# Performance work log

Measured on AMD Instinct MI355X. Metric: run time of the kernel, lower is better.

Reference implementation:

```python
import jax, jax.numpy as jnp
import numpy as np

B, S, HID = 4, 128, 4096
D, HQ, HK = 128, 32, 8
PAGES, PSIZE, NPP = 64, 256, 16  # page pool, page size, pages per sequence
THETA = 10000.0
EPS = 1e-6
SCALE = 1.0 / float(np.sqrt(D))


def setup_inputs() -> dict:
    key = jax.random.key(0)
    ks = jax.random.split(key, 10)
    x = jax.random.normal(ks[0], (B, S, HID), jnp.float32)
    Wq = jax.random.normal(ks[1], (HQ * D, HID), jnp.float32) * 0.02
    Wk = jax.random.normal(ks[2], (HK * D, HID), jnp.float32) * 0.02
    Wv = jax.random.normal(ks[3], (HK * D, HID), jnp.float32) * 0.02
    Wo = jax.random.normal(ks[4], (HID, HQ * D), jnp.float32) * 0.02
    q_norm_w = jax.random.uniform(ks[5], (D,), jnp.float32)
    k_norm_w = jax.random.uniform(ks[6], (D,), jnp.float32)
    k_cache = jax.random.normal(ks[7], (PAGES, PSIZE, HK, D), jnp.float32)
    v_cache = jax.random.normal(ks[8], (PAGES, PSIZE, HK, D), jnp.float32)
    block_table = jnp.arange(B * NPP, dtype=jnp.int32).reshape(B, NPP)
    cache_seqlens = jax.random.randint(ks[9], (B,), 0, 3800).astype(jnp.int32)
    return dict(x=x, Wq=Wq, Wk=Wk, Wv=Wv, Wo=Wo, q_norm_w=q_norm_w,
                k_norm_w=k_norm_w, k_cache=k_cache, v_cache=v_cache,
                block_table=block_table, cache_seqlens=cache_seqlens)


def _rmsnorm(t, w):
    # per-head RMSNorm over head_dim (constant_bias = 0)
    var = jnp.mean(t * t, axis=-1, keepdims=True)
    return t * jax.lax.rsqrt(var + EPS) * w


def _rope(t, pos):
    # NeoX-style half-rotation. t: [B,S,H,D], pos: [B,S]
    inv_freq = 1.0 / (THETA ** (jnp.arange(0, D, 2, dtype=jnp.float32) / D))  # [D/2]
    freqs = pos[..., None].astype(jnp.float32) * inv_freq                     # [B,S,D/2]
    cos = jnp.cos(freqs)[:, :, None, :]
    sin = jnp.sin(freqs)[:, :, None, :]
    t1, t2 = t[..., : D // 2], t[..., D // 2:]
    return jnp.concatenate([t1 * cos - t2 * sin, t2 * cos + t1 * sin], axis=-1)


def reference(x, Wq, Wk, Wv, Wo, q_norm_w, k_norm_w, k_cache, v_cache,
              block_table, cache_seqlens):
    bsz, seqlen, _ = x.shape
    # QKV projections
    q = jnp.einsum('bsd,ed->bse', x, Wq).reshape(bsz, seqlen, HQ, D)
    k = jnp.einsum('bsd,ed->bse', x, Wk).reshape(bsz, seqlen, HK, D)
    v = jnp.einsum('bsd,ed->bse', x, Wv).reshape(bsz, seqlen, HK, D)
    # QK-norm then RoPE (fused norm+rope path of the module)
    q = _rmsnorm(q, q_norm_w)
    k = _rmsnorm(k, k_norm_w)
    pos = cache_seqlens[:, None] + jnp.arange(seqlen)[None, :]  # [B,S]
    q = _rope(q, pos)
    k = _rope(k, pos)
    # Gather paged KV cache: [B, NPP*PSIZE, HK, D]
    L = NPP * PSIZE
    kc = k_cache[block_table].reshape(bsz, L, HK, D)
    vc = v_cache[block_table].reshape(bsz, L, HK, D)
    # Append new tokens (flash_attn_with_kvcache writes k,v into the cache)
    k_all = jnp.concatenate([kc, k], axis=1)  # [B, L+S, HK, D]
    v_all = jnp.concatenate([vc, v], axis=1)
    # Valid mask: cache slots < cache_seqlens; all new keys valid (causal=False, full window)
    valid_c = jnp.arange(L)[None, :] < cache_seqlens[:, None]          # [B, L]
    valid = jnp.concatenate(
        [valid_c, jnp.ones((bsz, seqlen), dtype=bool)], axis=1)        # [B, L+S]
    rep = HQ // HK
    k_all = jnp.repeat(k_all, rep, axis=2)
    v_all = jnp.repeat(v_all, rep, axis=2)
    scores = jnp.einsum('bqhd,bkhd->bhqk', q, k_all) * SCALE
    scores = jnp.where(valid[:, None, None, :], scores, -1e30)
    probs = jax.nn.softmax(scores, axis=-1)
    o = jnp.einsum('bhqk,bkhd->bqhd', probs, v_all)
    o = o.reshape(bsz, seqlen, HQ * D)
    return jnp.einsum('bse,de->bsd', o, Wo)
```

## Files before the change

### kernel.cpp

```cpp
#include <hip/hip_runtime.h>

typedef unsigned short u16;
typedef float f4v __attribute__((ext_vector_type(4)));
typedef short s8v __attribute__((ext_vector_type(8)));
typedef int   i4v __attribute__((ext_vector_type(4)));

#define SCALE_ 0.08838834764831845f
#define LOG2E_ 1.44269504088896340f

__device__ __forceinline__ u16 f2b(float f) {
    union { float f; unsigned u; } c; c.f = f;
    unsigned u = c.u + 0x7fffu + ((c.u >> 16) & 1u);
    return (u16)(u >> 16);
}

typedef const __attribute__((address_space(1))) unsigned int gu32;
typedef __attribute__((address_space(3))) unsigned int lu32;
__device__ __forceinline__ void glds16(const void* g, void* l) {
    __builtin_amdgcn_global_load_lds((gu32*)g, (lu32*)l, 16, 0, 0);
}

__device__ __forceinline__ int rho(int kv) {
    return (kv & 0x20) | ((kv & 0x04) << 2) | ((kv & 0x18) >> 1) | (kv & 3);
}

template <int RB>
__global__ __launch_bounds__(256) void wcvt_k(const float* __restrict__ src,
                                              u16* __restrict__ dst, int K) {
    const int kt = blockIdx.x, nt = blockIdx.y;
    u16* out = dst + ((size_t)nt * gridDim.x + kt) * (RB * 64);
#pragma unroll
    for (int i = 0; i < RB / 32; i++) {
        int c = threadIdx.x + i * 256;
        int r = c >> 3, c16 = c & 7, cc = c16 ^ (r & 7);
        const float* p = src + (size_t)(nt * RB + r) * K + kt * 64 + cc * 8;
        float4 f0 = *(const float4*)p, f1 = *(const float4*)(p + 4);
        s8v v;
        v[0] = (short)f2b(f0.x); v[1] = (short)f2b(f0.y);
        v[2] = (short)f2b(f0.z); v[3] = (short)f2b(f0.w);
        v[4] = (short)f2b(f1.x); v[5] = (short)f2b(f1.y);
        v[6] = (short)f2b(f1.z); v[7] = (short)f2b(f1.w);
        *(s8v*)(out + r * 64 + c16 * 8) = v;
    }
}

__global__ __launch_bounds__(256) void fgemm2(const u16* __restrict__ Ag,
                                              const u16* __restrict__ Bg,
                                              float* __restrict__ Cp,
                                              int M, int N, int K, int Ksl,
                                              int NY, int NZ) {
    __shared__ __align__(16) u16 As[2][4096];
    __shared__ __align__(16) u16 Bs[2][8192];
    const int tid = threadIdx.x, lane = tid & 63, wid = tid >> 6;
    const int lm = lane & 15, lg = lane >> 4;
    const int nb = gridDim.x, per = nb >> 3, w = blockIdx.x;
    const int idx = (w & 7) * per + (w >> 3);
    const int nx = idx / (NY * NZ);
    const int rem = idx - nx * (NY * NZ);
    const int my = rem % NY, z = rem / NY;
    const int m0 = my * 64, n0 = nx * 128;
    const int KT = K >> 6, NT = Ksl >> 6;
    const int kt0 = (z * Ksl) >> 6;
    const u16* ga = Ag + ((size_t)my * KT + kt0) * 4096;
    const u16* gb = Bg + ((size_t)nx * KT + kt0) * 8192;
    Cp += (size_t)z * M * N;

    f4v acc[4][2];
#pragma unroll
    for (int mi = 0; mi < 4; mi++)
#pragma unroll
        for (int ni = 0; ni < 2; ni++) acc[mi][ni] = (f4v){0.f, 0.f, 0.f, 0.f};

    auto STAGE = [&](int buf, int kt) {
        const char* a = (const char*)(ga + (size_t)kt * 4096) + tid * 16;
        const char* b = (const char*)(gb + (size_t)kt * 8192) + tid * 16;
        char* la = (char*)As[buf] + tid * 16;
        char* lb = (char*)Bs[buf] + tid * 16;
        glds16(a, la);
        glds16(a + 4096, la + 4096);
#pragma unroll
        for (int i = 0; i < 4; i++) glds16(b + i * 4096, lb + i * 4096);
    };

    STAGE(0, 0);
    asm volatile("s_waitcnt vmcnt(0)" ::: "memory");
    __syncthreads();

    for (int kt = 0; kt < NT; ++kt) {
        const int cur = kt & 1;
        if (kt + 1 < NT) STAGE(cur ^ 1, kt + 1);
#pragma unroll
        for (int ks = 0; ks < 2; ks++) {
            s8v av[4], bv[2];
#pragma unroll
            for (int mi = 0; mi < 4; mi++) {
                int r = mi * 16 + lm;
                av[mi] = *(const s8v*)(As[cur] + r * 64 + (((ks * 4 + lg) ^ (r & 7)) * 8));
            }
#pragma unroll
            for (int ni = 0; ni < 2; ni++) {
                int r = wid * 32 + ni * 16 + lm;
                bv[ni] = *(const s8v*)(Bs[cur] + r * 64 + (((ks * 4 + lg) ^ (r & 7)) * 8));
            }
#pragma unroll
            for (int mi = 0; mi < 4; mi++)
#pragma unroll
                for (int ni = 0; ni < 2; ni++)
                    acc[mi][ni] = __builtin_amdgcn_mfma_f32_16x16x32_bf16(av[mi], bv[ni], acc[mi][ni], 0, 0, 0);
        }
        asm volatile("s_waitcnt vmcnt(0)" ::: "memory");
        __syncthreads();
    }

#pragma unroll
    for (int mi = 0; mi < 4; mi++)
#pragma unroll
        for (int ni = 0; ni < 2; ni++)
#pragma unroll
            for (int r = 0; r < 4; r++) {
                int m = m0 + mi * 16 + lg * 4 + r;
                int n = n0 + wid * 32 + ni * 16 + lm;
                Cp[(size_t)m * N + n] = acc[mi][ni][r];
            }
}

__global__ __launch_bounds__(256) void nrope_k(const float* __restrict__ src,
                                               u16* __restrict__ dst,
                                               const float* __restrict__ w,
                                               const int* __restrict__ cseq,
                                               int nheads, float oscale,
                                               int nsl, size_t sls) {
    const int lane = threadIdx.x & 63;
    const int rid = blockIdx.x * 4 + (threadIdx.x >> 6);
    const int s = (rid / nheads) & 127;
    const int b = rid / (nheads * 128);
    const float* p = src + (size_t)rid * 128;
    float x1 = 0.f, x2 = 0.f;
    for (int sl = 0; sl < nsl; sl++) {
        x1 += p[sl * sls + lane];
        x2 += p[sl * sls + lane + 64];
    }
    float ss = x1 * x1 + x2 * x2;
#pragma unroll
    for (int off = 1; off < 64; off <<= 1) ss += __shfl_xor(ss, off);
    float inv = rsqrtf(ss * (1.0f / 128.0f) + 1e-6f);
    float n1 = x1 * inv * w[lane];
    float n2 = x2 * inv * w[lane + 64];
    float pos = (float)(cseq[b] + s);
    float ang = pos * powf(10000.0f, -(float)lane * (1.0f / 64.0f));
    float cs = cosf(ang), sn = sinf(ang);
    dst[(size_t)rid * 128 + lane]      = f2b((n1 * cs - n2 * sn) * oscale);
    dst[(size_t)rid * 128 + lane + 64] = f2b((n2 * cs + n1 * sn) * oscale);
}

__global__ __launch_bounds__(256) void cvt_bf16k(const float* __restrict__ s,
                                                 u16* __restrict__ d, int n4,
                                                 int nsl, size_t sls) {
    int i = blockIdx.x * blockDim.x + threadIdx.x;
    if (i < n4) {
        f4v f = (f4v){0.f, 0.f, 0.f, 0.f};
        for (int sl = 0; sl < nsl; sl++)
            f += *(const f4v*)(s + sl * sls + (size_t)i * 4);
        ushort4 o;
        o.x = f2b(f[0]); o.y = f2b(f[1]); o.z = f2b(f[2]); o.w = f2b(f[3]);
        ((ushort4*)d)[i] = o;
    }
}

__global__ __launch_bounds__(256) void red4_k(const float* __restrict__ p,
                                              float* __restrict__ out, int n4,
                                              size_t sls) {
    int i = blockIdx.x * blockDim.x + threadIdx.x;
    if (i < n4) {
        f4v s = (f4v){0.f, 0.f, 0.f, 0.f};
#pragma unroll
        for (int sl = 0; sl < 4; sl++)
            s += *(const f4v*)(p + sl * sls + (size_t)i * 4);
        *(f4v*)(out + (size_t)i * 4) = s;
    }
}

__global__ __launch_bounds__(256) void cvtkv_k(const float* __restrict__ kc,
                                               const float* __restrict__ vc,
                                               const u16* __restrict__ kb,
                                               const u16* __restrict__ vb,
                                               const int* __restrict__ btab,
                                               const int* __restrict__ cseq,
                                               u16* __restrict__ kb2,
                                               u16* __restrict__ vb2) {
    const int t = blockIdx.x, hk = blockIdx.y, b = blockIdx.z;
    const int tid = threadIdx.x;
    const int cl = cseq[b];
    if (t < 64 && t * 64 >= cl) return;
    u16* kout = kb2 + ((size_t)(b * 8 + hk) * 66 + t) * 8192;
    u16* vout = vb2 + ((size_t)(b * 8 + hk) * 66 + t) * 8192;

    if (t < 64) {
#pragma unroll
        for (int i = 0; i < 4; i++) {
            int c = tid + i * 256; int r = c >> 4, c16 = c & 15;
            int rs = rho(r);
            int cc = c16 ^ (rs & 7);
            int p = t * 64 + r;
            const float* src = kc + (((size_t)btab[b * 16 + (p >> 8)] * 256 + (p & 255)) * 8 + hk) * 128 + cc * 8;
            float4 f0 = *(const float4*)src, f1 = *(const float4*)(src + 4);
            s8v v;
            v[0] = (short)f2b(f0.x); v[1] = (short)f2b(f0.y); v[2] = (short)f2b(f0.z); v[3] = (short)f2b(f0.w);
            v[4] = (short)f2b(f1.x); v[5] = (short)f2b(f1.y); v[6] = (short)f2b(f1.z); v[7] = (short)f2b(f1.w);
            *(s8v*)(kout + rs * 128 + c16 * 8) = v;
        }
#pragma unroll
        for (int i = 0; i < 4; i++) {
            int c = tid + i * 256; int pr = c >> 5, c16v = c & 31;
            int nc = c16v ^ pr;
            int n = nc * 4;
            int p = t * 64 + pr * 2;
            const float* s0 = vc + (((size_t)btab[b * 16 + (p >> 8)] * 256 + (p & 255)) * 8 + hk) * 128 + n;
            float4 e = *(const float4*)s0, o = *(const float4*)(s0 + 1024);
            i4v w;
            w[0] = (int)((unsigned)f2b(e.x) | ((unsigned)f2b(o.x) << 16));
            w[1] = (int)((unsigned)f2b(e.y) | ((unsigned)f2b(o.y) << 16));
            w[2] = (int)((unsigned)f2b(e.z) | ((unsigned)f2b(o.z) << 16));
            w[3] = (int)((unsigned)f2b(e.w) | ((unsigned)f2b(o.w) << 16));
            *(i4v*)(vout + pr * 256 + c16v * 8) = w;
        }
    } else {
        int s0r = (t - 64) * 64;
#pragma unroll
        for (int i = 0; i < 4; i++) {
            int c = tid + i * 256; int r = c >> 4, c16 = c & 15;
            int rs = rho(r);
            int cc = c16 ^ (rs & 7);
            s8v v = *(const s8v*)(kb + ((size_t)(b * 128 + s0r + r) * 8 + hk) * 128 + cc * 8);
            *(s8v*)(kout + rs * 128 + c16 * 8) = v;
        }
#pragma unroll
        for (int i = 0; i < 4; i++) {
            int c = tid + i * 256; int pr = c >> 5, c16v = c & 31;
            int nc = c16v ^ pr;
            int n = nc * 4;
            const u16* s0 = vb + ((size_t)(b * 128 + s0r + pr * 2) * 8 + hk) * 128 + n;
            ushort4 e = *(const ushort4*)s0, o = *(const ushort4*)(s0 + 1024);
            i4v w;
            w[0] = (int)((unsigned)e.x | ((unsigned)o.x << 16));
            w[1] = (int)((unsigned)e.y | ((unsigned)o.y << 16));
            w[2] = (int)((unsigned)e.z | ((unsigned)o.z << 16));
            w[3] = (int)((unsigned)e.w | ((unsigned)o.w << 16));
            *(i4v*)(vout + pr * 256 + c16v * 8) = w;
        }
    }
}

__global__ __launch_bounds__(256) void fattn6_k(const u16* __restrict__ qb,
                                                const u16* __restrict__ kb2,
                                                const u16* __restrict__ vb2,
                                                const int* __restrict__ cseq,
                                                float* __restrict__ po,
                                                float* __restrict__ mb,
                                                float* __restrict__ lb) {
    __shared__ __align__(16) char Ks[2][8192];
    __shared__ __align__(16) char Vs[2][8192];

    const int tid = threadIdx.x, lane = tid & 63, wid = tid >> 6;
    const int lm = lane & 15, lg = lane >> 4;
    const int bid = blockIdx.x;
    const int sp = bid & 3, half = (bid >> 2) & 1, h = (bid >> 3) & 31, b = bid >> 8;
    const int hk = h >> 2;

    s8v qa[4];
    {
        const u16* qp = qb + ((size_t)((b * 128 + half * 64 + wid * 16 + lm) * 32 + h)) * 128 + lg * 8;
#pragma unroll
        for (int ks = 0; ks < 4; ks++) qa[ks] = *(const s8v*)(qp + ks * 32);
    }

    float m_run = -1e30f, l_run = 0.f;
    f4v acc[8];
#pragma unroll
    for (int dt = 0; dt < 8; dt++) acc[dt] = (f4v){0.f, 0.f, 0.f, 0.f};

    const int cl = cseq[b];
    const int ntc = (cl + 31) >> 5;
    const int tlo = (ntc * sp) >> 2, thi = (ntc * (sp + 1)) >> 2;
    const int ncache = thi - tlo;
    const int ntiles = ncache + (sp == 3 ? 4 : 0);

    const char* gk = (const char*)kb2 + (size_t)(b * 8 + hk) * 66 * 16384;
    const char* gv = (const char*)vb2 + (size_t)(b * 8 + hk) * 66 * 16384;

    auto STAGE = [&](int buf, int gt) {
        const char* gkt = gk + (size_t)gt * 8192 + tid * 16;
        const char* gvt = gv + (size_t)gt * 8192 + tid * 16;
        char* lk = Ks[buf] + tid * 16;
        char* lv = Vs[buf] + tid * 16;
        glds16(gkt, lk);
        glds16(gkt + 4096, lk + 4096);
        glds16(gvt, lv);
        glds16(gvt + 4096, lv + 4096);
    };
    auto GT = [&](int ii) { return ii < ncache ? tlo + ii : 128 + (ii - ncache); };

    if (ntiles > 0) STAGE(0, GT(0));
    asm volatile("s_waitcnt vmcnt(0)" ::: "memory");
    __syncthreads();

    for (int ii = 0; ii < ntiles; ++ii) {
        const int cur = ii & 1;
        if (ii + 1 < ntiles) STAGE(cur ^ 1, GT(ii + 1));
        const int gt = GT(ii);
        const int t0 = gt * 32;

        f4v sc[2];
#pragma unroll
        for (int ct = 0; ct < 2; ct++) sc[ct] = (f4v){0.f, 0.f, 0.f, 0.f};
        __builtin_amdgcn_s_setprio(1);
#pragma unroll
        for (int ct = 0; ct < 2; ct++) {
#pragma unroll
            for (int ks = 0; ks < 4; ks++) {
                int r = ct * 16 + lm;
                s8v kf = *(const s8v*)(Ks[cur] + ((r * 256 + ks * 64 + lg * 16) ^ ((r & 7) << 4)));
                sc[ct] = __builtin_amdgcn_mfma_f32_16x16x32_bf16(kf, qa[ks], sc[ct], 0, 0, 0);
            }
        }
        __builtin_amdgcn_s_setprio(0);

        if (gt < 128 && (t0 + 32 > cl)) {
#pragma unroll
            for (int ct = 0; ct < 2; ct++)
#pragma unroll
                for (int r = 0; r < 4; r++) {
                    int kvloc = lg * 8 + ct * 4 + r;
                    if (t0 + kvloc >= cl) sc[ct][r] = -1e30f;
                }
        }

        float mt = fmaxf(fmaxf(fmaxf(sc[0][0], sc[0][1]), fmaxf(sc[0][2], sc[0][3])),
                         fmaxf(fmaxf(sc[1][0], sc[1][1]), fmaxf(sc[1][2], sc[1][3])));
        mt = fmaxf(mt, __shfl_xor(mt, 16));
        mt = fmaxf(mt, __shfl_xor(mt, 32));

        if (__any(mt > m_run + 12.0f)) {
            float mn = fmaxf(m_run, mt);
            float corr = exp2f(m_run - mn);
            m_run = mn;
            l_run *= corr;
            float c0 = __shfl(corr, lg * 4 + 0);
            float c1 = __shfl(corr, lg * 4 + 1);
            float c2 = __shfl(corr, lg * 4 + 2);
            float c3 = __shfl(corr, lg * 4 + 3);
#pragma unroll
            for (int dt = 0; dt < 8; dt++) {
                acc[dt][0] *= c0; acc[dt][1] *= c1;
                acc[dt][2] *= c2; acc[dt][3] *= c3;
            }
        }

        short pb[2][4];
        float ladd = 0.f;
#pragma unroll
        for (int ct = 0; ct < 2; ct++)
#pragma unroll
            for (int r = 0; r < 4; r++) {
                float pv = exp2f(sc[ct][r] - m_run);
                ladd += pv;
                pb[ct][r] = (short)f2b(pv);
            }
        l_run += ladd;

        __builtin_amdgcn_s_setprio(1);
        {
            s8v pa;
#pragma unroll
            for (int j = 0; j < 4; j++) { pa[j] = pb[0][j]; pa[4 + j] = pb[1][j]; }
            const int pko = (gt & 1) << 4;
#pragma unroll
            for (int dt = 0; dt < 8; dt++) {
                i4v vv;
#pragma unroll
                for (int t = 0; t < 4; t++) {
                    int p = lg * 4 + t;
                    vv[t] = *(const int*)(Vs[cur] + p * 512 + ((((dt * 16 + lm) * 4)) ^ (((p + pko) & 31) << 4)));
                }
                union { i4v i; s8v s; } u; u.i = vv;
                acc[dt] = __builtin_amdgcn_mfma_f32_16x16x32_bf16(pa, u.s, acc[dt], 0, 0, 0);
            }
        }
        __builtin_amdgcn_s_setprio(0);

        asm volatile("s_waitcnt vmcnt(0)" ::: "memory");
        __syncthreads();
    }

#pragma unroll
    for (int dt = 0; dt < 8; dt++) {
#pragma unroll
        for (int r = 0; r < 4; r++) {
            int row = wid * 16 + lg * 4 + r;
            po[((size_t)bid * 64 + row) * 128 + dt * 16 + lm] = acc[dt][r];
        }
    }
    float lt = l_run;
    lt += __shfl_xor(lt, 16);
    lt += __shfl_xor(lt, 32);
    if (lg == 0) {
        mb[(size_t)bid * 64 + wid * 16 + lm] = m_run;
        lb[(size_t)bid * 64 + wid * 16 + lm] = lt;
    }
}

__global__ __launch_bounds__(256) void fcomb_k(const float* __restrict__ po,
                                               const float* __restrict__ mb,
                                               const float* __restrict__ lb,
                                               u16* __restrict__ obT) {
    const int pid = blockIdx.x, t = threadIdx.x;
    const int row = t >> 2, dq = t & 3;
    const int half = pid & 1, h = (pid >> 1) & 31, b = pid >> 6;
    float m[4], l[4];
#pragma unroll
    for (int i = 0; i < 4; i++) {
        m[i] = mb[(size_t)(pid * 4 + i) * 64 + row];
        l[i] = lb[(size_t)(pid * 4 + i) * 64 + row];
    }
    float M = fmaxf(fmaxf(m[0], m[1]), fmaxf(m[2], m[3]));
    float w[4], L = 0.f;
#pragma unroll
    for (int i = 0; i < 4; i++) { w[i] = exp2f(m[i] - M); L += w[i] * l[i]; }
    float invL = 1.0f / L;
    const int arow = b * 128 + half * 64 + row;
    const int mt = arow >> 6, rr = arow & 63;
#pragma unroll
    for (int j = 0; j < 8; j++) {
        f4v s = (f4v){0.f, 0.f, 0.f, 0.f};
#pragma unroll
        for (int i = 0; i < 4; i++) {
            f4v a = *(const f4v*)(po + ((size_t)(pid * 4 + i) * 64 + row) * 128 + dq * 32 + j * 4);
            s += w[i] * a;
        }
        ushort4 o;
        o.x = f2b(s[0] * invL); o.y = f2b(s[1] * invL);
        o.z = f2b(s[2] * invL); o.w = f2b(s[3] * invL);
        const int acol = h * 128 + dq * 32 + j * 4;
        const int kt = acol >> 6, cch = (acol >> 3) & 7, wo = acol & 7;
        *(ushort4*)(obT + ((size_t)(mt * 64 + kt)) * 4096 + rr * 64 + ((cch ^ (rr & 7)) * 8) + wo) = o;
    }
}

extern "C" void kernel_launch(void* const* d_in, const int* in_sizes, int n_in,
                              void* d_out, int out_size, void* d_ws, size_t ws_size,
                              hipStream_t stream) {
    const float* x   = (const float*)d_in[0];
    const float* Wq  = (const float*)d_in[1];
    const float* Wk  = (const float*)d_in[2];
    const float* Wv  = (const float*)d_in[3];
    const float* Wo  = (const float*)d_in[4];
    const float* qnw = (const float*)d_in[5];
    const float* knw = (const float*)d_in[6];
    const float* kc  = (const float*)d_in[7];
    const float* vc  = (const float*)d_in[8];
    const int* btab  = (const int*)d_in[9];
    const int* cseq  = (const int*)d_in[10];
    float* out = (float*)d_out;

    char* ws = (char*)d_ws;
    u16*   qb   = (u16*)(ws + 0);
    u16*   kb   = (u16*)(ws + 4194304);
    u16*   vb   = (u16*)(ws + 5242880);
    u16*   obT  = (u16*)(ws + 6291456);
    u16*   xb   = (u16*)(ws + 6291456);
    float* mbuf = (float*)(ws + 10485760);
    float* lbuf = (float*)(ws + 10747904);
    float* P    = (float*)(ws + 11010048);
    u16*   wW   = (u16*)(ws + 44564480);
    u16*   kb2  = (u16*)(ws + 44564480);
    u16*   vb2  = (u16*)(ws + 79167488);

    dim3 blk(256, 1, 1);
    const size_t slsQ = (size_t)512 * 4096, slsKV = (size_t)512 * 1024;

    wcvt_k<64><<<dim3(64, 8, 1), blk, 0, stream>>>(x, xb, 4096);

    wcvt_k<128><<<dim3(64, 32, 1), blk, 0, stream>>>(Wq, wW, 4096);
    fgemm2<<<dim3(1024, 1, 1), blk, 0, stream>>>(xb, wW, P, 512, 4096, 4096, 1024, 8, 4);
    nrope_k<<<dim3(4096, 1, 1), blk, 0, stream>>>(P, qb, qnw, cseq, 32, SCALE_ * LOG2E_, 4, slsQ);

    wcvt_k<128><<<dim3(64, 8, 1), blk, 0, stream>>>(Wk, wW, 4096);
    fgemm2<<<dim3(512, 1, 1), blk, 0, stream>>>(xb, wW, P, 512, 1024, 4096, 512, 8, 8);
    nrope_k<<<dim3(1024, 1, 1), blk, 0, stream>>>(P, kb, knw, cseq, 8, 1.0f, 8, slsKV);

    wcvt_k<128><<<dim3(64, 8, 1), blk, 0, stream>>>(Wv, wW, 4096);
    fgemm2<<<dim3(512, 1, 1), blk, 0, stream>>>(xb, wW, P, 512, 1024, 4096, 512, 8, 8);
    cvt_bf16k<<<dim3(512, 1, 1), blk, 0, stream>>>(P, vb, 131072, 8, slsKV);

    cvtkv_k<<<dim3(66, 8, 4), blk, 0, stream>>>(kc, vc, kb, vb, btab, cseq, kb2, vb2);
    fattn6_k<<<dim3(1024, 1, 1), blk, 0, stream>>>(qb, kb2, vb2, cseq, P, mbuf, lbuf);
    fcomb_k<<<dim3(256, 1, 1), blk, 0, stream>>>(P, mbuf, lbuf, obT);

    wcvt_k<128><<<dim3(64, 32, 1), blk, 0, stream>>>(Wo, wW, 4096);
    fgemm2<<<dim3(1024, 1, 1), blk, 0, stream>>>(obT, wW, P, 512, 4096, 4096, 1024, 8, 4);
    red4_k<<<dim3(2048, 1, 1), blk, 0, stream>>>(P, out, 2097152, slsQ);
}
```

Before: 259.6 us.

## Fuse Q/K/V projections into one GEMM with merged weight convert and epilogue

Merges the three separate weight conversions into one kernel that writes Wq, Wk and Wv into a single concatenated bf16 buffer. A single split-K GEMM with N=6144 then produces Q, K and V together, using 2 K-slices instead of 4 or 8, which cuts the partial-sum traffic. One epilogue kernel applies RMSNorm+RoPE to Q and K and converts V, replacing three launches. This reduces kernel launches and fp32 partial writes, at the cost of changing the grid/split-K balance of the GEMM and needing more workspace for the wider output.

```diff
diff --git a/kernel.cpp b/kernel.cpp
--- a/kernel.cpp
+++ b/kernel.cpp
@@ -34,6 +34,32 @@
         int c = threadIdx.x + i * 256;
         int r = c >> 3, c16 = c & 7, cc = c16 ^ (r & 7);
         const float* p = src + (size_t)(nt * RB + r) * K + kt * 64 + cc * 8;
+        float4 f0 = *(const float4*)p, f1 = *(const float4*)(p + 4);
+        s8v v;
+        v[0] = (short)f2b(f0.x); v[1] = (short)f2b(f0.y);
+        v[2] = (short)f2b(f0.z); v[3] = (short)f2b(f0.w);
+        v[4] = (short)f2b(f1.x); v[5] = (short)f2b(f1.y);
+        v[6] = (short)f2b(f1.z); v[7] = (short)f2b(f1.w);
+        *(s8v*)(out + r * 64 + c16 * 8) = v;
+    }
+}
+
+__global__ __launch_bounds__(256) void wcvt3_k(const float* __restrict__ Wq,
+                                               const float* __restrict__ Wk,
+                                               const float* __restrict__ Wv,
+                                               u16* __restrict__ dst, int K) {
+    const int kt = blockIdx.x, nt = blockIdx.y;
+    const float* src;
+    int ln;
+    if (nt < 32)      { src = Wq; ln = nt; }
+    else if (nt < 40) { src = Wk; ln = nt - 32; }
+    else              { src = Wv; ln = nt - 40; }
+    u16* out = dst + ((size_t)nt * gridDim.x + kt) * 8192;
+#pragma unroll
+    for (int i = 0; i < 4; i++) {
+        int c = threadIdx.x + i * 256;
+        int r = c >> 3, c16 = c & 7, cc = c16 ^ (r & 7);
+        const float* p = src + (size_t)(ln * 128 + r) * K + kt * 64 + cc * 8;
         float4 f0 = *(const float4*)p, f1 = *(const float4*)(p + 4);
         s8v v;
         v[0] = (short)f2b(f0.x); v[1] = (short)f2b(f0.y);
@@ -124,46 +150,62 @@
             }
 }
 
-__global__ __launch_bounds__(256) void nrope_k(const float* __restrict__ src,
-                                               u16* __restrict__ dst,
-                                               const float* __restrict__ w,
-                                               const int* __restrict__ cseq,
-                                               int nheads, float oscale,
-                                               int nsl, size_t sls) {
-    const int lane = threadIdx.x & 63;
-    const int rid = blockIdx.x * 4 + (threadIdx.x >> 6);
-    const int s = (rid / nheads) & 127;
-    const int b = rid / (nheads * 128);
-    const float* p = src + (size_t)rid * 128;
-    float x1 = 0.f, x2 = 0.f;
-    for (int sl = 0; sl < nsl; sl++) {
-        x1 += p[sl * sls + lane];
-        x2 += p[sl * sls + lane + 64];
-    }
-    float ss = x1 * x1 + x2 * x2;
-#pragma unroll
-    for (int off = 1; off < 64; off <<= 1) ss += __shfl_xor(ss, off);
-    float inv = rsqrtf(ss * (1.0f / 128.0f) + 1e-6f);
-    float n1 = x1 * inv * w[lane];
-    float n2 = x2 * inv * w[lane + 64];
-    float pos = (float)(cseq[b] + s);
-    float ang = pos * powf(10000.0f, -(float)lane * (1.0f / 64.0f));
-    float cs = cosf(ang), sn = sinf(ang);
-    dst[(size_t)rid * 128 + lane]      = f2b((n1 * cs - n2 * sn) * oscale);
-    dst[(size_t)rid * 128 + lane + 64] = f2b((n2 * cs + n1 * sn) * oscale);
-}
-
-__global__ __launch_bounds__(256) void cvt_bf16k(const float* __restrict__ s,
-                                                 u16* __restrict__ d, int n4,
-                                                 int nsl, size_t sls) {
-    int i = blockIdx.x * blockDim.x + threadIdx.x;
-    if (i < n4) {
-        f4v f = (f4v){0.f, 0.f, 0.f, 0.f};
-        for (int sl = 0; sl < nsl; sl++)
-            f += *(const f4v*)(s + sl * sls + (size_t)i * 4);
-        ushort4 o;
-        o.x = f2b(f[0]); o.y = f2b(f[1]); o.z = f2b(f[2]); o.w = f2b(f[3]);
-        ((ushort4*)d)[i] = o;
+__global__ __launch_bounds__(256) void epi_k(const float* __restrict__ C,
+                                             u16* __restrict__ qb,
+                                             u16* __restrict__ kb,
+                                             u16* __restrict__ vb,
+                                             const float* __restrict__ qnw,
+                                             const float* __restrict__ knw,
+                                             const int* __restrict__ cseq) {
+    const int lane = threadIdx.x & 63, w = threadIdx.x >> 6;
+    const int blk = blockIdx.x;
+    const size_t sls = (size_t)512 * 6144;
+
+    if (blk < 4096) {
+        const int rid = blk * 4 + w;
+        const int h = rid & 31, m = rid >> 5;
+        const int s = m & 127, b = m >> 7;
+        const float* p = C + (size_t)m * 6144 + h * 128;
+        float x1 = p[lane] + p[sls + lane];
+        float x2 = p[lane + 64] + p[sls + lane + 64];
+        float ss = x1 * x1 + x2 * x2;
+#pragma unroll
+        for (int off = 1; off < 64; off <<= 1) ss += __shfl_xor(ss, off);
+        float inv = rsqrtf(ss * (1.0f / 128.0f) + 1e-6f);
+        float n1 = x1 * inv * qnw[lane];
+        float n2 = x2 * inv * qnw[lane + 64];
+        float pos = (float)(cseq[b] + s);
+        float ang = pos * powf(10000.0f, -(float)lane * (1.0f / 64.0f));
+        float cs = cosf(ang), sn = sinf(ang);
+        const float osc = SCALE_ * LOG2E_;
+        qb[(size_t)rid * 128 + lane]      = f2b((n1 * cs - n2 * sn) * osc);
+        qb[(size_t)rid * 128 + lane + 64] = f2b((n2 * cs + n1 * sn) * osc);
+    } else if (blk < 5120) {
+        const int rid = (blk - 4096) * 4 + w;
+        const int hk = rid & 7, m = rid >> 3;
+        const int s = m & 127, b = m >> 7;
+        const float* p = C + (size_t)m * 6144 + 4096 + hk * 128;
+        float x1 = p[lane] + p[sls + lane];
+        float x2 = p[lane + 64] + p[sls + lane + 64];
+        float ss = x1 * x1 + x2 * x2;
+#pragma unroll
+        for (int off = 1; off < 64; off <<= 1) ss += __shfl_xor(ss, off);
+        float inv = rsqrtf(ss * (1.0f / 128.0f) + 1e-6f);
+        float n1 = x1 * inv * knw[lane];
+        float n2 = x2 * inv * knw[lane + 64];
+        float pos = (float)(cseq[b] + s);
+        float ang = pos * powf(10000.0f, -(float)lane * (1.0f / 64.0f));
+        float cs = cosf(ang), sn = sinf(ang);
+        kb[(size_t)rid * 128 + lane]      = f2b(n1 * cs - n2 * sn);
+        kb[(size_t)rid * 128 + lane + 64] = f2b(n2 * cs + n1 * sn);
+    } else {
+        const int rid = (blk - 5120) * 4 + w;
+        const int hk = rid & 7, m = rid >> 3;
+        const float* p = C + (size_t)m * 6144 + 5120 + hk * 128;
+        float x1 = p[lane] + p[sls + lane];
+        float x2 = p[lane + 64] + p[sls + lane + 64];
+        vb[(size_t)rid * 128 + lane]      = f2b(x1);
+        vb[(size_t)rid * 128 + lane + 64] = f2b(x2);
     }
 }
 
@@ -476,21 +518,11 @@
     u16*   vb2  = (u16*)(ws + 79167488);
 
     dim3 blk(256, 1, 1);
-    const size_t slsQ = (size_t)512 * 4096, slsKV = (size_t)512 * 1024;
 
     wcvt_k<64><<<dim3(64, 8, 1), blk, 0, stream>>>(x, xb, 4096);
-
-    wcvt_k<128><<<dim3(64, 32, 1), blk, 0, stream>>>(Wq, wW, 4096);
-    fgemm2<<<dim3(1024, 1, 1), blk, 0, stream>>>(xb, wW, P, 512, 4096, 4096, 1024, 8, 4);
-    nrope_k<<<dim3(4096, 1, 1), blk, 0, stream>>>(P, qb, qnw, cseq, 32, SCALE_ * LOG2E_, 4, slsQ);
-
-    wcvt_k<128><<<dim3(64, 8, 1), blk, 0, stream>>>(Wk, wW, 4096);
-    fgemm2<<<dim3(512, 1, 1), blk, 0, stream>>>(xb, wW, P, 512, 1024, 4096, 512, 8, 8);
-    nrope_k<<<dim3(1024, 1, 1), blk, 0, stream>>>(P, kb, knw, cseq, 8, 1.0f, 8, slsKV);
-
-    wcvt_k<128><<<dim3(64, 8, 1), blk, 0, stream>>>(Wv, wW, 4096);
-    fgemm2<<<dim3(512, 1, 1), blk, 0, stream>>>(xb, wW, P, 512, 1024, 4096, 512, 8, 8);
-    cvt_bf16k<<<dim3(512, 1, 1), blk, 0, stream>>>(P, vb, 131072, 8, slsKV);
+    wcvt3_k<<<dim3(64, 48, 1), blk, 0, stream>>>(Wq, Wk, Wv, wW, 4096);
+    fgemm2<<<dim3(768, 1, 1), blk, 0, stream>>>(xb, wW, P, 512, 6144, 4096, 2048, 8, 2);
+    epi_k<<<dim3(6144, 1, 1), blk, 0, stream>>>(P, qb, kb, vb, qnw, knw, cseq);
 
     cvtkv_k<<<dim3(66, 8, 4), blk, 0, stream>>>(kc, vc, kb, vb, btab, cseq, kb2, vb2);
     fattn6_k<<<dim3(1024, 1, 1), blk, 0, stream>>>(qb, kb2, vb2, cseq, P, mbuf, lbuf);
@@ -498,5 +530,5 @@
 
     wcvt_k<128><<<dim3(64, 32, 1), blk, 0, stream>>>(Wo, wW, 4096);
     fgemm2<<<dim3(1024, 1, 1), blk, 0, stream>>>(obT, wW, P, 512, 4096, 4096, 1024, 8, 4);
-    red4_k<<<dim3(2048, 1, 1), blk, 0, stream>>>(P, out, 2097152, slsQ);
-}
+    red4_k<<<dim3(2048, 1, 1), blk, 0, stream>>>(P, out, 2097152, (size_t)512 * 4096);
+}
```

Result: faster. 218.4 us (-15.9%).
